# Kernel optimization log

Hardware: AMD Instinct MI355X
Metric: run time of the kernel (lower is better)

Reference implementation:

```python
import jax, jax.numpy as jnp
import numpy as np

B, N, D = 8, 9856, 256
HEADS = 8
WH, WW = 7, 11
HID = 512  # int(D * 2.0)
EPS = 1e-5


def layernorm(x, g, b):
    mu = jnp.mean(x, axis=-1, keepdims=True)
    var = jnp.mean(jnp.square(x - mu), axis=-1, keepdims=True)
    return (x - mu) * jax.lax.rsqrt(var + EPS) * g + b


def setup_inputs() -> dict:
    key = jax.random.key(0)
    ks = jax.random.split(key, 6)
    s = lambda k, shape: (jax.random.normal(k, shape, jnp.float32) * 0.02)
    return {
        "x": jax.random.normal(ks[0], (B, N, D), jnp.float32),
        "norm1_g": jnp.ones((D,), jnp.float32),
        "norm1_b": jnp.zeros((D,), jnp.float32),
        "in_proj_w": s(ks[1], (3 * D, D)),
        "in_proj_b": jnp.zeros((3 * D,), jnp.float32),
        "out_w": s(ks[2], (D, D)),
        "out_b": jnp.zeros((D,), jnp.float32),
        "norm2_g": jnp.ones((D,), jnp.float32),
        "norm2_b": jnp.zeros((D,), jnp.float32),
        "fc1_w": s(ks[3], (HID, D)),
        "fc1_b": jnp.zeros((HID,), jnp.float32),
        "fc2_w": s(ks[4], (D, HID)),
        "fc2_b": jnp.zeros((D,), jnp.float32),
        "h": 56,
        "w": 176,
    }


def reference(x, norm1_g, norm1_b, in_proj_w, in_proj_b, out_w, out_b,
              norm2_g, norm2_b, fc1_w, fc1_b, fc2_w, fc2_b, h, w):
    Bx, Nx, Dx = x.shape
    n_h, n_w = h // WH, w // WW  # chosen dims divide evenly -> pad_h = pad_w = 0
    hd = Dx // HEADS
    L = WH * WW  # 77 tokens per window

    res = x
    xn = layernorm(x, norm1_g, norm1_b)

    # window partition: (B, h*w, D) -> (B*n_h*n_w, wh*ww, D)
    win = xn.reshape(Bx, n_h, WH, n_w, WW, Dx)
    win = win.transpose(0, 1, 3, 2, 4, 5).reshape(-1, L, Dx)

    # MultiheadAttention (batch_first) on each window independently
    qkv = win @ in_proj_w.T + in_proj_b          # (NW, L, 3D)
    q, k, v = jnp.split(qkv, 3, axis=-1)
    NW = win.shape[0]
    q = q.reshape(NW, L, HEADS, hd).transpose(0, 2, 1, 3)
    k = k.reshape(NW, L, HEADS, hd).transpose(0, 2, 1, 3)
    v = v.reshape(NW, L, HEADS, hd).transpose(0, 2, 1, 3)
    scores = jnp.einsum("nhld,nhmd->nhlm", q, k) / jnp.sqrt(jnp.float32(hd))
    attn = jax.nn.softmax(scores, axis=-1)
    o = jnp.einsum("nhlm,nhmd->nhld", attn, v)   # (NW, H, L, hd)
    o = o.transpose(0, 2, 1, 3).reshape(NW, L, Dx)
    o = o @ out_w.T + out_b

    # window reverse: (B*n_h*n_w, wh*ww, D) -> (B, h*w, D)
    o = o.reshape(Bx, n_h, n_w, WH, WW, Dx)
    o = o.transpose(0, 1, 3, 2, 4, 5).reshape(Bx, Nx, Dx)

    x = res + o
    res = x
    xn2 = layernorm(x, norm2_g, norm2_b)
    hmid = jax.nn.gelu(xn2 @ fc1_w.T + fc1_b, approximate=False)
    mlp = hmid @ fc2_w.T + fc2_b
    return res + mlp
```

## Files before the change

kernel.cpp:

```cpp
#include <hip/hip_runtime.h>
#include <hip/hip_bf16.h>

typedef unsigned short u16;
typedef unsigned int   u32;

typedef __bf16 bf16x8 __attribute__((ext_vector_type(8)));
typedef float  f32x4  __attribute__((ext_vector_type(4)));

__device__ __forceinline__ u16 f2bf(float f) {
  u32 u = __float_as_uint(f);
  u += 0x7fffu + ((u >> 16) & 1u);
  return (u16)(u >> 16);
}
__device__ __forceinline__ u32 pack2(float a, float b) {
  return (u32)f2bf(a) | ((u32)f2bf(b) << 16);
}
__device__ __forceinline__ void gld16(const void* g, void* l) {
  __builtin_amdgcn_global_load_lds(
      (const __attribute__((address_space(1))) unsigned int*)g,
      (__attribute__((address_space(3))) unsigned int*)l, 16, 0, 0);
}

#define TOK_M   78848
#define DIM     256
#define NWIN    1024
#define WINL    77

template<int K, int NF>
__device__ __forceinline__ void cvt_chunk(const float* __restrict__ src,
                                          u16* __restrict__ dst, int rel)
{
  constexpr int KT = K / 32;
  constexpr int PN = NF * 16;
  const int lane  = rel & 63;
  const int g     = rel >> 6;
  const int nf    = g % NF;
  const int kt    = (g / NF) % KT;
  const int panel = g / (NF * KT);
  const int col   = panel * PN + nf * 16 + (lane & 15);
  const int k0    = kt * 32 + (lane >> 4) * 8;
  const float4 a = *(const float4*)(src + (size_t)col * K + k0);
  const float4 b = *(const float4*)(src + (size_t)col * K + k0 + 4);
  uint4 o;
  o.x = pack2(a.x, a.y); o.y = pack2(a.z, a.w);
  o.z = pack2(b.x, b.y); o.w = pack2(b.z, b.w);
  *(uint4*)(dst + (size_t)rel * 8) = o;
}
__device__ __forceinline__ void cvt_plain(const float* __restrict__ src,
                                          u16* __restrict__ dst, int rel)
{
  const int i = rel * 8;
  const float4 a = *(const float4*)(src + i);
  const float4 b = *(const float4*)(src + i + 4);
  uint4 o;
  o.x = pack2(a.x, a.y); o.y = pack2(a.z, a.w);
  o.z = pack2(b.x, b.y); o.w = pack2(b.z, b.w);
  *(uint4*)(dst + i) = o;
}

__global__ __launch_bounds__(256)
void cvt_w(const float* __restrict__ wqkv, const float* __restrict__ wout,
           const float* __restrict__ w1, const float* __restrict__ w2,
           u16* __restrict__ out)
{
  const int c = blockIdx.x * 256 + threadIdx.x;
  if      (c < 24576) cvt_chunk<256, 8>(wqkv, out,          c);
  else if (c < 32768) cvt_plain(wout, out + 196608, c - 24576);
  else if (c < 49152) cvt_chunk<256, 8>(w1,   out + 262144, c - 32768);
  else                cvt_plain(w2,   out + 393216, c - 49152);
}

template<int NPAN, int EPI, int OBF, int PERM>
__global__ __launch_bounds__(256, 3)
void lngemm(const float* __restrict__ X, const u16* __restrict__ Wimg,
            const float* __restrict__ lg, const float* __restrict__ lb,
            const float* __restrict__ bias, void* __restrict__ Cout)
{
  constexpr int K  = 256;
  constexpr int KT = K / 32;
  constexpr int N  = NPAN * 128;
  __shared__ u16 At[64 * K];
  __shared__ u16 Bs[2][4096];

  const int tid  = threadIdx.x;
  const int wave = tid >> 6, lane = tid & 63;
  const int quad = lane >> 4, l16 = lane & 15;
  const int wy = wave >> 1, wx = wave & 1;
  const int rowbase = blockIdx.x * 64;

  {
    const float4 gg = *(const float4*)(lg + lane * 4);
    const float4 bb = *(const float4*)(lb + lane * 4);
    const int c  = lane * 4;
    const int kt = c >> 5, kb = (c >> 3) & 3, ko = c & 7;
    for (int r = 0; r < 16; ++r) {
      const int row = wave * 16 + r;
      const float4 v = *(const float4*)(X + (size_t)(rowbase + row) * 256 + c);
      float s = v.x + v.y + v.z + v.w;
#pragma unroll
      for (int off = 32; off; off >>= 1) s += __shfl_xor(s, off);
      const float mu = s * (1.f / 256.f);
      const float dx = v.x - mu, dy = v.y - mu, dz = v.z - mu, dw = v.w - mu;
      float q = dx * dx + dy * dy + dz * dz + dw * dw;
#pragma unroll
      for (int off = 32; off; off >>= 1) q += __shfl_xor(q, off);
      const float rstd = rsqrtf(q * (1.f / 256.f) + 1e-5f);
      uint2 o;
      o.x = pack2(dx * rstd * gg.x + bb.x, dy * rstd * gg.y + bb.y);
      o.y = pack2(dz * rstd * gg.z + bb.z, dw * rstd * gg.w + bb.w);
      *(uint2*)(At + row * 256 + kt * 32 + ((kb ^ (row & 3)) * 8) + ko) = o;
    }
  }
  gld16(Wimg + tid * 8,        Bs[0] + tid * 8);
  gld16(Wimg + 2048 + tid * 8, Bs[0] + 2048 + tid * 8);
  __syncthreads();

  int step = 0;
  for (int np = 0; np < NPAN; ++np) {
    f32x4 acc[2][4];
#pragma unroll
    for (int mi = 0; mi < 2; ++mi)
#pragma unroll
      for (int ni = 0; ni < 4; ++ni) {
        f32x4 z = {0.f, 0.f, 0.f, 0.f};
        acc[mi][ni] = z;
      }
#pragma unroll
    for (int kt = 0; kt < KT; ++kt, ++step) {
      const int cur = step & 1;
      if (step + 1 < NPAN * KT) {
        const u16* src = Wimg + (size_t)(step + 1) * 4096;
        gld16(src + tid * 8,        Bs[cur ^ 1] + tid * 8);
        gld16(src + 2048 + tid * 8, Bs[cur ^ 1] + 2048 + tid * 8);
      }
      bf16x8 af[2], bv[4];
#pragma unroll
      for (int mi = 0; mi < 2; ++mi)
        af[mi] = *(const bf16x8*)(At + (wy * 32 + mi * 16 + l16) * 256 +
                                  kt * 32 + (quad ^ (l16 & 3)) * 8);
#pragma unroll
      for (int ni = 0; ni < 4; ++ni)
        bv[ni] = *(const bf16x8*)(Bs[cur] + ((wx * 4 + ni) * 64 + lane) * 8);
#pragma unroll
      for (int mi = 0; mi < 2; ++mi)
#pragma unroll
        for (int ni = 0; ni < 4; ++ni)
          acc[mi][ni] = __builtin_amdgcn_mfma_f32_16x16x32_bf16(
              af[mi], bv[ni], acc[mi][ni], 0, 0, 0);
      __syncthreads();
    }
    const int col0 = np * 128 + wx * 64 + l16;
#pragma unroll
    for (int mi = 0; mi < 2; ++mi) {
      const int r = rowbase + wy * 32 + mi * 16 + quad * 4;
#pragma unroll
      for (int e = 0; e < 4; ++e) {
        const int gr = r + e;
        size_t orow = (size_t)gr;
        if (PERM) {
          const int b  = gr / 9856, n = gr - b * 9856;
          const int y  = n / 176,  xc = n - y * 176;
          const int ih = y / 7,    rr = y - ih * 7;
          const int iw = xc / 11,  cc = xc - iw * 11;
          orow = (size_t)(((b * 8 + ih) * 16 + iw)) * 77 + rr * 11 + cc;
        }
#pragma unroll
        for (int ni = 0; ni < 4; ++ni) {
          const int col = col0 + ni * 16;
          float v = acc[mi][ni][e] + bias[col];
          if (EPI == 2) v = 0.5f * v * (1.f + erff(v * 0.70710678118654752f));
          const size_t idx = orow * N + col;
          if (OBF) ((u16*)Cout)[idx] = f2bf(v);
          else     ((float*)Cout)[idx] = v;
        }
      }
    }
  }
}

template<int EPI, int OBF>
__global__ __launch_bounds__(256, 3)
void gemm_mfma(const u16* __restrict__ A, const u16* __restrict__ W,
               const float* __restrict__ bias, const float* res,
               void* Cout, int N, int K)
{
  __shared__ u16 As[2][4096];
  __shared__ u16 Bs[2][4096];

  const int tid  = threadIdx.x;
  const int wave = tid >> 6, lane = tid & 63;
  const int wy = wave >> 1, wx = wave & 1;
  const int quad = lane >> 4, l16 = lane & 15;
  const int m0 = blockIdx.y * 128;
  const int n0 = blockIdx.x * 128;

  const int s0 = tid, s1 = tid + 256;
  const int r0 = s0 >> 2, r1 = s1 >> 2;
  const int kb0 = (s0 & 3) ^ (r0 & 3);
  const int kb1 = (s1 & 3) ^ (r1 & 3);
  const u16* Ag0 = A + (size_t)(m0 + r0) * K + kb0 * 8;
  const u16* Ag1 = A + (size_t)(m0 + r1) * K + kb1 * 8;
  const u16* Bg0 = W + (size_t)(n0 + r0) * K + kb0 * 8;
  const u16* Bg1 = W + (size_t)(n0 + r1) * K + kb1 * 8;

  const int kbs = quad ^ (l16 & 3);
  const int aoff = (wy * 64 + l16) * 32 + kbs * 8;
  const int boff = (wx * 64 + l16) * 32 + kbs * 8;

  f32x4 acc[4][4];
#pragma unroll
  for (int i = 0; i < 4; ++i)
#pragma unroll
    for (int j = 0; j < 4; ++j) {
      f32x4 z = {0.f, 0.f, 0.f, 0.f};
      acc[i][j] = z;
    }

  gld16(Ag0, &As[0][s0 * 8]);
  gld16(Ag1, &As[0][s1 * 8]);
  gld16(Bg0, &Bs[0][s0 * 8]);
  gld16(Bg1, &Bs[0][s1 * 8]);
  __syncthreads();

  const int NT = K >> 5;
  for (int t = 0; t < NT; ++t) {
    const int cur = t & 1;
    if (t + 1 < NT) {
      const int kt = (t + 1) << 5;
      gld16(Ag0 + kt, &As[cur ^ 1][s0 * 8]);
      gld16(Ag1 + kt, &As[cur ^ 1][s1 * 8]);
      gld16(Bg0 + kt, &Bs[cur ^ 1][s0 * 8]);
      gld16(Bg1 + kt, &Bs[cur ^ 1][s1 * 8]);
    }
    const u16* Ar = &As[cur][aoff];
    const u16* Br = &Bs[cur][boff];
    bf16x8 af[4], bv[4];
#pragma unroll
    for (int i = 0; i < 4; ++i) {
      af[i] = *(const bf16x8*)(Ar + i * 16 * 32);
      bv[i] = *(const bf16x8*)(Br + i * 16 * 32);
    }
#pragma unroll
    for (int mi = 0; mi < 4; ++mi)
#pragma unroll
      for (int ni = 0; ni < 4; ++ni)
        acc[mi][ni] = __builtin_amdgcn_mfma_f32_16x16x32_bf16(
            af[mi], bv[ni], acc[mi][ni], 0, 0, 0);
    __syncthreads();
  }

  const int gr0 = m0 + wy * 64 + quad * 4;
  const int gc0 = n0 + wx * 64 + l16;
#pragma unroll
  for (int ni = 0; ni < 4; ++ni) {
    const int gc = gc0 + ni * 16;
    const float bvs = bias[gc];
#pragma unroll
    for (int mi = 0; mi < 4; ++mi) {
      const int gr = gr0 + mi * 16;
      f32x4 a = acc[mi][ni];
#pragma unroll
      for (int e = 0; e < 4; ++e) {
        float v = a[e] + bvs;
        const size_t idx = (size_t)(gr + e) * N + gc;
        if (EPI == 1) v += res[idx];
        else if (EPI == 2) v = 0.5f * v * (1.f + erff(v * 0.70710678118654752f));
        if (OBF) ((u16*)Cout)[idx] = f2bf(v);
        else     ((float*)Cout)[idx] = v;
      }
    }
  }
}

#define PSTR 104
__global__ __launch_bounds__(128)
void attn_mfma(const u16* __restrict__ qkv, u16* __restrict__ onat)
{
  __shared__ __bf16 Pb[2][80 * PSTR];

  const int tid  = threadIdx.x;
  const int wave = tid >> 6, lane = tid & 63;
  const int quad = lane >> 4, l16 = lane & 15;
  const int pair = blockIdx.x * 2 + wave;
  const int nw   = pair >> 3, head = pair & 7;
  const size_t base = (size_t)nw * 77 * 768;
  const int hoff = head * 32;
  __bf16* P = Pb[wave];

  {
    uint4 z = {0, 0, 0, 0};
    for (int r = lane; r < 80; r += 64) {
      *(uint4*)(P + r * PSTR + 80) = z;
      *(uint4*)(P + r * PSTR + 88) = z;
    }
  }

  bf16x8 qf[5], kf[5];
  const u16* qp = qkv + base + hoff + quad * 8;
#pragma unroll
  for (int mi = 0; mi < 5; ++mi) {
    const size_t row = (size_t)(l16 + 16 * mi) * 768;
    qf[mi] = *(const bf16x8*)(qp + row);
    kf[mi] = *(const bf16x8*)(qp + row + 256);
  }

  f32x4 s[5][5];
#pragma unroll
  for (int mi = 0; mi < 5; ++mi)
#pragma unroll
    for (int ni = 0; ni < 5; ++ni) {
      f32x4 z = {0.f, 0.f, 0.f, 0.f};
      s[mi][ni] = z;
    }
#pragma unroll
  for (int mi = 0; mi < 5; ++mi)
#pragma unroll
    for (int ni = 0; ni < 5; ++ni)
      s[mi][ni] = __builtin_amdgcn_mfma_f32_16x16x32_bf16(
          qf[mi], kf[ni], s[mi][ni], 0, 0, 0);

  bf16x8 vf[3][2];
  {
    const __bf16* vbb = (const __bf16*)(qkv + base + 512 + hoff + l16);
#pragma unroll
    for (int ks = 0; ks < 3; ++ks)
#pragma unroll
      for (int ni = 0; ni < 2; ++ni)
#pragma unroll
        for (int jj = 0; jj < 8; ++jj) {
          const int k = ks * 32 + quad * 8 + jj;
          vf[ks][ni][jj] = (k < 77) ? vbb[(size_t)k * 768 + 16 * ni] : (__bf16)0.f;
        }
  }

  if (l16 >= 13) {
#pragma unroll
    for (int mi = 0; mi < 5; ++mi)
#pragma unroll
      for (int e = 0; e < 4; ++e) s[mi][4][e] = -1e30f;
  }

  const float c = 0.17677669529663687f * 1.4426950408889634f;
  float inv[5][4];
#pragma unroll
  for (int mi = 0; mi < 5; ++mi)
#pragma unroll
    for (int e = 0; e < 4; ++e) {
      float mx = s[mi][0][e];
#pragma unroll
      for (int ni = 1; ni < 5; ++ni) mx = fmaxf(mx, s[mi][ni][e]);
#pragma unroll
      for (int off = 1; off < 16; off <<= 1) mx = fmaxf(mx, __shfl_xor(mx, off));
      float sum = 0.f;
#pragma unroll
      for (int ni = 0; ni < 5; ++ni) {
        const float ev = exp2f((s[mi][ni][e] - mx) * c);
        s[mi][ni][e] = ev;
        sum += ev;
      }
#pragma unroll
      for (int off = 1; off < 16; off <<= 1) sum += __shfl_xor(sum, off);
      inv[mi][e] = 1.f / sum;
    }

#pragma unroll
  for (int mi = 0; mi < 5; ++mi)
#pragma unroll
    for (int e = 0; e < 4; ++e) {
      const int m = quad * 4 + e + 16 * mi;
#pragma unroll
      for (int ni = 0; ni < 5; ++ni)
        P[m * PSTR + l16 + 16 * ni] = (__bf16)(s[mi][ni][e] * inv[mi][e]);
    }

  f32x4 o[5][2];
#pragma unroll
  for (int mi = 0; mi < 5; ++mi)
#pragma unroll
    for (int ni = 0; ni < 2; ++ni) {
      f32x4 z = {0.f, 0.f, 0.f, 0.f};
      o[mi][ni] = z;
    }
#pragma unroll
  for (int ks = 0; ks < 3; ++ks)
#pragma unroll
    for (int mi = 0; mi < 5; ++mi) {
      const bf16x8 af = *(const bf16x8*)(P + (l16 + 16 * mi) * PSTR + ks * 32 + quad * 8);
#pragma unroll
      for (int ni = 0; ni < 2; ++ni)
        o[mi][ni] = __builtin_amdgcn_mfma_f32_16x16x32_bf16(
            af, vf[ks][ni], o[mi][ni], 0, 0, 0);
    }

  const int b  = nw >> 7;
  const int ih = (nw >> 4) & 7;
  const int iw = nw & 15;
#pragma unroll
  for (int mi = 0; mi < 5; ++mi)
#pragma unroll
    for (int e = 0; e < 4; ++e) {
      const int t = quad * 4 + e + 16 * mi;
      if (t < 77) {
        const int rr = t / 11, cc = t - rr * 11;
        const int y = ih * 7 + rr, xc = iw * 11 + cc;
        const size_t nat = (size_t)b * 9856 + (size_t)y * 176 + xc;
        u16* dst = onat + nat * DIM + hoff + l16;
        dst[0]  = f2bf(o[mi][0][e]);
        dst[16] = f2bf(o[mi][1][e]);
      }
    }
}

extern "C" void kernel_launch(void* const* d_in, const int* in_sizes, int n_in,
                              void* d_out, int out_size, void* d_ws, size_t ws_size,
                              hipStream_t stream)
{
  (void)in_sizes; (void)n_in; (void)out_size; (void)ws_size;
  const float* x    = (const float*)d_in[0];
  const float* g1   = (const float*)d_in[1];
  const float* b1   = (const float*)d_in[2];
  const float* wqkv = (const float*)d_in[3];
  const float* bqkv = (const float*)d_in[4];
  const float* wout = (const float*)d_in[5];
  const float* bout = (const float*)d_in[6];
  const float* g2   = (const float*)d_in[7];
  const float* b2   = (const float*)d_in[8];
  const float* w1   = (const float*)d_in[9];
  const float* bf1  = (const float*)d_in[10];
  const float* w2   = (const float*)d_in[11];
  const float* bf2  = (const float*)d_in[12];

  char* ws = (char*)d_ws;
  u16*   qkv  = (u16*)(ws);
  u16*   onat = (u16*)(ws + 161480704);
  u16*   wb   = (u16*)(ws + 201850880);
  u16*   wqkv_b = wb;
  u16*   wout_b = wb + 196608;
  u16*   w1_b   = wb + 262144;
  u16*   w2_b   = wb + 393216;
  float* x2   = (float*)d_out;

  cvt_w<<<256, 256, 0, stream>>>(wqkv, wout, w1, w2, wb);
  lngemm<6, 0, 1, 1><<<1232, 256, 0, stream>>>(x, wqkv_b, g1, b1, bqkv, qkv);
  attn_mfma<<<4096, 128, 0, stream>>>(qkv, onat);
  gemm_mfma<1, 0><<<dim3(2, 616), 256, 0, stream>>>(onat, wout_b, bout, x, x2, 256, 256);
  lngemm<4, 2, 1, 0><<<1232, 256, 0, stream>>>(x2, w1_b, g2, b2, bf1, qkv);
  gemm_mfma<1, 0><<<dim3(2, 616), 256, 0, stream>>>(qkv, w2_b, bf2, x2, x2, 256, 512);
}
```

Baseline: 575.0 us.

## Deepen GEMM weight/activation prefetch to 4-stage ring with one barrier per step

Both the LayerNorm-fused GEMM and the plain MFMA GEMM move from a double buffer to a 4-slot LDS ring that prefetches two K-tiles ahead. They use explicit vmcnt waits and a single barrier per iteration instead of a trailing __syncthreads. The LDS swizzle changes to an XOR over more row bits to reduce bank conflicts, and the LN prologue issues all row loads before reducing. Launch bounds drop to 2 blocks per CU because of the larger LDS footprint, which lowers occupancy.

```diff
diff --git a/kernel.cpp b/kernel.cpp
--- a/kernel.cpp
+++ b/kernel.cpp
@@ -71,7 +71,7 @@
 }
 
 template<int NPAN, int EPI, int OBF, int PERM>
-__global__ __launch_bounds__(256, 3)
+__global__ __launch_bounds__(256, 2)
 void lngemm(const float* __restrict__ X, const u16* __restrict__ Wimg,
             const float* __restrict__ lg, const float* __restrict__ lb,
             const float* __restrict__ bias, void* __restrict__ Cout)
@@ -79,8 +79,9 @@
   constexpr int K  = 256;
   constexpr int KT = K / 32;
   constexpr int N  = NPAN * 128;
+  constexpr int NSTEP = NPAN * KT;
   __shared__ u16 At[64 * K];
-  __shared__ u16 Bs[2][4096];
+  __shared__ u16 Bs[4][4096];
 
   const int tid  = threadIdx.x;
   const int wave = tid >> 6, lane = tid & 63;
@@ -91,11 +92,15 @@
   {
     const float4 gg = *(const float4*)(lg + lane * 4);
     const float4 bb = *(const float4*)(lb + lane * 4);
-    const int c  = lane * 4;
-    const int kt = c >> 5, kb = (c >> 3) & 3, ko = c & 7;
+    const int c = lane * 4;
+    float4 xv[16];
+#pragma unroll
+    for (int r = 0; r < 16; ++r)
+      xv[r] = *(const float4*)(X + (size_t)(rowbase + wave * 16 + r) * 256 + c);
+#pragma unroll
     for (int r = 0; r < 16; ++r) {
       const int row = wave * 16 + r;
-      const float4 v = *(const float4*)(X + (size_t)(rowbase + row) * 256 + c);
+      const float4 v = xv[r];
       float s = v.x + v.y + v.z + v.w;
 #pragma unroll
       for (int off = 32; off; off >>= 1) s += __shfl_xor(s, off);
@@ -108,12 +113,13 @@
       uint2 o;
       o.x = pack2(dx * rstd * gg.x + bb.x, dy * rstd * gg.y + bb.y);
       o.y = pack2(dz * rstd * gg.z + bb.z, dw * rstd * gg.w + bb.w);
-      *(uint2*)(At + row * 256 + kt * 32 + ((kb ^ (row & 3)) * 8) + ko) = o;
+      *(uint2*)(At + row * 256 + (c ^ ((row & 7) * 8))) = o;
     }
   }
   gld16(Wimg + tid * 8,        Bs[0] + tid * 8);
   gld16(Wimg + 2048 + tid * 8, Bs[0] + 2048 + tid * 8);
-  __syncthreads();
+  gld16(Wimg + 4096 + tid * 8,        Bs[1] + tid * 8);
+  gld16(Wimg + 4096 + 2048 + tid * 8, Bs[1] + 2048 + tid * 8);
 
   int step = 0;
   for (int np = 0; np < NPAN; ++np) {
@@ -127,27 +133,32 @@
       }
 #pragma unroll
     for (int kt = 0; kt < KT; ++kt, ++step) {
-      const int cur = step & 1;
-      if (step + 1 < NPAN * KT) {
-        const u16* src = Wimg + (size_t)(step + 1) * 4096;
-        gld16(src + tid * 8,        Bs[cur ^ 1] + tid * 8);
-        gld16(src + 2048 + tid * 8, Bs[cur ^ 1] + 2048 + tid * 8);
-      }
+      {
+        const int sn = (step + 2 < NSTEP) ? step + 2 : NSTEP - 1;
+        const u16* src = Wimg + (size_t)sn * 4096;
+        u16* dst = Bs[(step + 2) & 3];
+        gld16(src + tid * 8,        dst + tid * 8);
+        gld16(src + 2048 + tid * 8, dst + 2048 + tid * 8);
+      }
+      asm volatile("s_waitcnt vmcnt(4) lgkmcnt(0)" ::: "memory");
+      __builtin_amdgcn_s_barrier();
+      __builtin_amdgcn_sched_barrier(0);
       bf16x8 af[2], bv[4];
 #pragma unroll
-      for (int mi = 0; mi < 2; ++mi)
-        af[mi] = *(const bf16x8*)(At + (wy * 32 + mi * 16 + l16) * 256 +
-                                  kt * 32 + (quad ^ (l16 & 3)) * 8);
+      for (int mi = 0; mi < 2; ++mi) {
+        const int row = wy * 32 + mi * 16 + l16;
+        af[mi] = *(const bf16x8*)(At + row * 256 +
+                                  ((kt * 32 + quad * 8) ^ ((row & 7) * 8)));
+      }
 #pragma unroll
       for (int ni = 0; ni < 4; ++ni)
-        bv[ni] = *(const bf16x8*)(Bs[cur] + ((wx * 4 + ni) * 64 + lane) * 8);
+        bv[ni] = *(const bf16x8*)(Bs[step & 3] + ((wx * 4 + ni) * 64 + lane) * 8);
 #pragma unroll
       for (int mi = 0; mi < 2; ++mi)
 #pragma unroll
         for (int ni = 0; ni < 4; ++ni)
           acc[mi][ni] = __builtin_amdgcn_mfma_f32_16x16x32_bf16(
               af[mi], bv[ni], acc[mi][ni], 0, 0, 0);
-      __syncthreads();
     }
     const int col0 = np * 128 + wx * 64 + l16;
 #pragma unroll
@@ -179,13 +190,13 @@
 }
 
 template<int EPI, int OBF>
-__global__ __launch_bounds__(256, 3)
+__global__ __launch_bounds__(256, 2)
 void gemm_mfma(const u16* __restrict__ A, const u16* __restrict__ W,
                const float* __restrict__ bias, const float* res,
                void* Cout, int N, int K)
 {
-  __shared__ u16 As[2][4096];
-  __shared__ u16 Bs[2][4096];
+  __shared__ u16 As[4][4096];
+  __shared__ u16 Bs[4][4096];
 
   const int tid  = threadIdx.x;
   const int wave = tid >> 6, lane = tid & 63;
@@ -196,14 +207,14 @@
 
   const int s0 = tid, s1 = tid + 256;
   const int r0 = s0 >> 2, r1 = s1 >> 2;
-  const int kb0 = (s0 & 3) ^ (r0 & 3);
-  const int kb1 = (s1 & 3) ^ (r1 & 3);
+  const int kb0 = (s0 & 3) ^ ((r0 >> 1) & 3);
+  const int kb1 = (s1 & 3) ^ ((r1 >> 1) & 3);
   const u16* Ag0 = A + (size_t)(m0 + r0) * K + kb0 * 8;
   const u16* Ag1 = A + (size_t)(m0 + r1) * K + kb1 * 8;
   const u16* Bg0 = W + (size_t)(n0 + r0) * K + kb0 * 8;
   const u16* Bg1 = W + (size_t)(n0 + r1) * K + kb1 * 8;
 
-  const int kbs = quad ^ (l16 & 3);
+  const int kbs = quad ^ ((l16 >> 1) & 3);
   const int aoff = (wy * 64 + l16) * 32 + kbs * 8;
   const int boff = (wx * 64 + l16) * 32 + kbs * 8;
 
@@ -216,24 +227,24 @@
       acc[i][j] = z;
     }
 
-  gld16(Ag0, &As[0][s0 * 8]);
-  gld16(Ag1, &As[0][s1 * 8]);
-  gld16(Bg0, &Bs[0][s0 * 8]);
-  gld16(Bg1, &Bs[0][s1 * 8]);
-  __syncthreads();
-
   const int NT = K >> 5;
+  auto stage = [&](int tile, int buf) {
+    const int ko = tile * 32;
+    gld16(Ag0 + ko, &As[buf][s0 * 8]);
+    gld16(Ag1 + ko, &As[buf][s1 * 8]);
+    gld16(Bg0 + ko, &Bs[buf][s0 * 8]);
+    gld16(Bg1 + ko, &Bs[buf][s1 * 8]);
+  };
+  stage(0, 0);
+  stage(1, 1);
+
   for (int t = 0; t < NT; ++t) {
-    const int cur = t & 1;
-    if (t + 1 < NT) {
-      const int kt = (t + 1) << 5;
-      gld16(Ag0 + kt, &As[cur ^ 1][s0 * 8]);
-      gld16(Ag1 + kt, &As[cur ^ 1][s1 * 8]);
-      gld16(Bg0 + kt, &Bs[cur ^ 1][s0 * 8]);
-      gld16(Bg1 + kt, &Bs[cur ^ 1][s1 * 8]);
-    }
-    const u16* Ar = &As[cur][aoff];
-    const u16* Br = &Bs[cur][boff];
+    stage((t + 2 < NT) ? t + 2 : NT - 1, (t + 2) & 3);
+    asm volatile("s_waitcnt vmcnt(8) lgkmcnt(0)" ::: "memory");
+    __builtin_amdgcn_s_barrier();
+    __builtin_amdgcn_sched_barrier(0);
+    const u16* Ar = &As[t & 3][aoff];
+    const u16* Br = &Bs[t & 3][boff];
     bf16x8 af[4], bv[4];
 #pragma unroll
     for (int i = 0; i < 4; ++i) {
@@ -246,7 +257,6 @@
       for (int ni = 0; ni < 4; ++ni)
         acc[mi][ni] = __builtin_amdgcn_mfma_f32_16x16x32_bf16(
             af[mi], bv[ni], acc[mi][ni], 0, 0, 0);
-    __syncthreads();
   }
 
   const int gr0 = m0 + wy * 64 + quad * 4;
```

Result: no change. 582.0 us (+1.2%).
